# Performance work log

Measured on AMD Instinct MI355X. Metric: run time of the kernel, lower is better.

The kernel has to match this reference:

```python
import jax, jax.numpy as jnp
import numpy as np

N_NODES = 100000
N_EDGES = 1000000
IN_DIM = 64
HID_DIM = 64


def _gcn_conv(x, W, b, rows, cols, deg_inv_sqrt):
    # x: [N, Fin] -> [N, Fout]; rows/cols already include self-loops
    xw = x @ W                                   # [N, Fout]
    norm = deg_inv_sqrt[rows] * deg_inv_sqrt[cols]  # [E+N]
    msg = xw[cols] * norm[:, None]               # gather + scale, [E+N, Fout]
    out = jax.ops.segment_sum(msg, rows, num_segments=x.shape[0])  # scatter-add
    return out + b


def _prelu(x, a):
    return jnp.where(x >= 0, x, a * x)


def _encode(x, edge_index, perm, W1, b1, prelu_a, W2, b2):
    N = x.shape[0]
    loops = jnp.arange(N, dtype=edge_index.dtype)
    rows = jnp.concatenate([edge_index[0], loops])
    cols = jnp.concatenate([edge_index[1], loops])
    deg = jax.ops.segment_sum(jnp.ones_like(rows, dtype=x.dtype), rows, num_segments=N)
    dis = jnp.where(deg > 0, jax.lax.rsqrt(deg), 0.0)

    def enc(feat):
        h = _gcn_conv(feat, W1, b1, rows, cols, dis)
        h = _prelu(h, prelu_a)
        return _gcn_conv(h, W2, b2, rows, cols, dis)

    positive = enc(x)
    negative = enc(x[perm])  # corruption: row permutation of features
    summary = jax.nn.sigmoid(positive.mean(axis=0))
    return positive, negative, summary


def setup_inputs() -> dict:
    key = jax.random.key(0)
    kx, ke, kp, k1, k2 = jax.random.split(key, 5)
    x = jax.random.normal(kx, (N_NODES, IN_DIM), dtype=jnp.float32)
    edge_index = jax.random.randint(ke, (2, N_EDGES), 0, N_NODES, dtype=jnp.int32)
    perm = jax.random.permutation(kp, N_NODES).astype(jnp.int32)
    s1 = 1.0 / np.sqrt(IN_DIM)
    s2 = 1.0 / np.sqrt(HID_DIM)
    W1 = jax.random.uniform(k1, (IN_DIM, HID_DIM), jnp.float32, -s1, s1)
    b1 = jnp.zeros((HID_DIM,), jnp.float32)
    W2 = jax.random.uniform(k2, (HID_DIM, HID_DIM), jnp.float32, -s2, s2)
    b2 = jnp.zeros((HID_DIM,), jnp.float32)
    prelu_a = jnp.float32(0.25)
    return {"x": x, "edge_index": edge_index, "perm": perm,
            "W1": W1, "b1": b1, "prelu_a": prelu_a, "W2": W2, "b2": b2}


def reference(x, edge_index, perm, W1, b1, prelu_a, W2, b2):
    return _encode(x, edge_index, perm, W1, b1, prelu_a, W2, b2)
```

## Files before the change

### kernel.cpp

```cpp
#include <hip/hip_runtime.h>
#include <hip/hip_fp16.h>
#include <math.h>

namespace {

constexpr int NN = 100000;
constexpr int NE = 1000000;
constexpr int D  = 64;

constexpr int RPB_LOG = 8;
constexpr int RPB = 1 << RPB_LOG;
constexpr int NBUK = (NN + RPB - 1) >> RPB_LOG;
constexpr int CAP = 4096;
constexpr int TILE = 2048;
constexpr int NTILES = (NE + TILE - 1) / TILE;

using ushort_t = unsigned short;
typedef __attribute__((ext_vector_type(8))) short short8;
typedef __attribute__((ext_vector_type(4))) float f32x4;

union FragU { uint4 v; short8 s; };

__device__ inline void split2(float f0, float f1, unsigned int& hi, unsigned int& lo) {
    unsigned int u0 = __float_as_uint(f0);
    unsigned int u1 = __float_as_uint(f1);
    hi = (u0 >> 16) | (u1 & 0xffff0000u);
    float l0 = f0 - __uint_as_float(u0 & 0xffff0000u);
    float l1 = f1 - __uint_as_float(u1 & 0xffff0000u);
    lo = (__float_as_uint(l0) >> 16) | (__float_as_uint(l1) & 0xffff0000u);
}

__device__ inline unsigned int packh(float a, float b) {
    union { __half2 h; unsigned int u; } cv;
    cv.h = __float22half2_rn(make_float2(a, b));
    return cv.u;
}

__device__ inline float2 h2f(unsigned int v) {
    union { unsigned int u; __half2 h; } cv;
    cv.u = v;
    return __half22float2(cv.h);
}

__global__ void binw_k(const int* __restrict__ rows, const int* __restrict__ cols,
                       int* __restrict__ bcount, unsigned int* __restrict__ binned, int e,
                       const float* __restrict__ W1, const float* __restrict__ W2,
                       uint4* __restrict__ fb) {
    __shared__ int hist[NBUK];
    __shared__ int gbase[NBUK];
    __shared__ int lofs[NBUK];
    if (blockIdx.x == NTILES) {
        int lane = threadIdx.x;
        if (lane < 64) {
            for (int w = 0; w < 2; ++w) {
                const float* W = (w != 0) ? W2 : W1;
                uint4* out = fb + w * 1024;
                for (int ft = 0; ft < 4; ++ft) {
                    for (int kt = 0; kt < 2; ++kt) {
                        int m  = ft * 16 + (lane & 15);
                        int k0 = kt * 32 + (lane >> 4) * 8;
                        unsigned int hi0, lo0, hi1, lo1, hi2, lo2, hi3, lo3;
                        split2(W[(k0 + 0) * 64 + m], W[(k0 + 1) * 64 + m], hi0, lo0);
                        split2(W[(k0 + 2) * 64 + m], W[(k0 + 3) * 64 + m], hi1, lo1);
                        split2(W[(k0 + 4) * 64 + m], W[(k0 + 5) * 64 + m], hi2, lo2);
                        split2(W[(k0 + 6) * 64 + m], W[(k0 + 7) * 64 + m], hi3, lo3);
                        out[((ft * 2 + kt) * 2 + 0) * 64 + lane] = make_uint4(hi0, hi1, hi2, hi3);
                        out[((ft * 2 + kt) * 2 + 1) * 64 + lane] = make_uint4(lo0, lo1, lo2, lo3);
                    }
                }
            }
        }
        return;
    }
    int base = blockIdx.x * TILE;
    for (int i = threadIdx.x; i < NBUK; i += blockDim.x) {
        hist[i] = 0;
        lofs[i] = 0;
    }
    __syncthreads();
    int r[8];
    int c[8];
    int bk[8];
#pragma unroll
    for (int j = 0; j < 8; ++j) {
        int i = base + j * 256 + threadIdx.x;
        if (i < e) {
            r[j] = rows[i];
            c[j] = cols[i];
            bk[j] = r[j] >> RPB_LOG;
            atomicAdd(&hist[bk[j]], 1);
        } else {
            bk[j] = -1;
        }
    }
    __syncthreads();
    for (int b = threadIdx.x; b < NBUK; b += blockDim.x) {
        int h = hist[b];
        gbase[b] = h ? atomicAdd(&bcount[b], h) : 0;
    }
    __syncthreads();
#pragma unroll
    for (int j = 0; j < 8; ++j) {
        if (bk[j] >= 0) {
            int l = gbase[bk[j]] + atomicAdd(&lofs[bk[j]], 1);
            if (l < CAP) {
                unsigned int v = ((unsigned int)(r[j] & (RPB - 1)) << 17) | (unsigned int)c[j];
                binned[(size_t)bk[j] * CAP + l] = v;
            }
        }
    }
}

__global__ void bucket_sort_k(const unsigned int* __restrict__ binned,
                              const int* __restrict__ bcount,
                              int* __restrict__ scols, int* __restrict__ rowstart,
                              int* __restrict__ deg, float* __restrict__ dis) {
    __shared__ int lcur[RPB];
    __shared__ int srs[RPB];
    __shared__ int wsum[8];
    __shared__ int redpart[8];
    __shared__ int sbase;
    int b = blockIdx.x;
    int row0 = b << RPB_LOG;
    int nrows = min(RPB, NN - row0);
    int cnt = bcount[b];
    const unsigned int* src = binned + (size_t)b * CAP;
    int tid = threadIdx.x;
    int lane = tid & 63;
    int wid = tid >> 6;

    int bv = (tid < NBUK && tid < b) ? bcount[tid] : 0;
    int bs = bv;
#pragma unroll
    for (int off = 1; off < 64; off <<= 1) {
        bs += __shfl_xor(bs, off, 64);
    }
    if (lane == 0) redpart[wid] = bs;
    __syncthreads();
    if (tid == 0) {
        int t = 0;
        for (int w = 0; w < 8; ++w) t += redpart[w];
        sbase = t;
    }
    if (tid < RPB) {
        lcur[tid] = 0;
    }
    __syncthreads();
    int bb = sbase;

    for (int i = tid; i < cnt; i += blockDim.x) {
        atomicAdd(&lcur[src[i] >> 17], 1);
    }
    __syncthreads();
    int d = (tid < nrows) ? lcur[tid] : 0;
    int inc = d;
#pragma unroll
    for (int off = 1; off < 64; off <<= 1) {
        int t = __shfl_up(inc, off);
        if (lane >= off) inc += t;
    }
    if (lane == 63) wsum[wid] = inc;
    __syncthreads();
    int wpre = 0;
    for (int w = 0; w < wid; ++w) wpre += wsum[w];
    int gstart = bb + wpre + inc - d;
    if (tid < nrows) {
        rowstart[row0 + tid] = gstart;
        deg[row0 + tid] = d;
        dis[row0 + tid] = rsqrtf((float)(d + 1));
    }
    __syncthreads();
    if (tid < RPB) {
        srs[tid] = gstart;
        lcur[tid] = 0;
    }
    __syncthreads();
    for (int i = tid; i < cnt; i += blockDim.x) {
        unsigned int v = src[i];
        int rl = (int)(v >> 17);
        int pos = srs[rl] + atomicAdd(&lcur[rl], 1);
        scols[pos] = (int)(v & 0x1FFFFu);
    }
}

__global__ void gemm1_k(const float* __restrict__ in, const uint4* __restrict__ wf,
                        ushort_t* __restrict__ tPN, const int* __restrict__ perm,
                        const float* __restrict__ dis, int n) {
    int lane  = threadIdx.x & 63;
    int wtile = (int)((blockIdx.x * blockDim.x + threadIdx.x) >> 6);
    if (wtile * 16 >= n) return;
    int node = wtile * 16 + (lane & 15);
    int kg   = lane >> 4;

    FragU whi[4][2];
    FragU wlo[4][2];
#pragma unroll
    for (int ft = 0; ft < 4; ++ft) {
#pragma unroll
        for (int kt = 0; kt < 2; ++kt) {
            whi[ft][kt].v = wf[((ft * 2 + kt) * 2 + 0) * 64 + lane];
            wlo[ft][kt].v = wf[((ft * 2 + kt) * 2 + 1) * 64 + lane];
        }
    }

    const float4* xr = (const float4*)in;
    size_t rbase = (size_t)node * 16 + (size_t)(kg * 2);
    int pnode = perm[node];
    size_t pbase = (size_t)pnode * 16 + (size_t)(kg * 2);
    f32x4 accP[4];
    f32x4 accN[4];
#pragma unroll
    for (int ft = 0; ft < 4; ++ft) {
        accP[ft] = f32x4{0.f, 0.f, 0.f, 0.f};
        accN[ft] = f32x4{0.f, 0.f, 0.f, 0.f};
    }
#pragma unroll
    for (int kt = 0; kt < 2; ++kt) {
        float4 a0 = xr[rbase + kt * 8];
        float4 a1 = xr[rbase + kt * 8 + 1];
        float4 g0 = xr[pbase + kt * 8];
        float4 g1 = xr[pbase + kt * 8 + 1];
        unsigned int h0, l0, h1, l1, h2, l2, h3, l3;
        split2(a0.x, a0.y, h0, l0);
        split2(a0.z, a0.w, h1, l1);
        split2(a1.x, a1.y, h2, l2);
        split2(a1.z, a1.w, h3, l3);
        FragU xhiP, xloP;
        xhiP.v = make_uint4(h0, h1, h2, h3);
        xloP.v = make_uint4(l0, l1, l2, l3);
        split2(g0.x, g0.y, h0, l0);
        split2(g0.z, g0.w, h1, l1);
        split2(g1.x, g1.y, h2, l2);
        split2(g1.z, g1.w, h3, l3);
        FragU xhiN, xloN;
        xhiN.v = make_uint4(h0, h1, h2, h3);
        xloN.v = make_uint4(l0, l1, l2, l3);
#pragma unroll
        for (int ft = 0; ft < 4; ++ft) {
            accP[ft] = __builtin_amdgcn_mfma_f32_16x16x32_bf16(whi[ft][kt].s, xhiP.s, accP[ft], 0, 0, 0);
            accP[ft] = __builtin_amdgcn_mfma_f32_16x16x32_bf16(whi[ft][kt].s, xloP.s, accP[ft], 0, 0, 0);
            accP[ft] = __builtin_amdgcn_mfma_f32_16x16x32_bf16(wlo[ft][kt].s, xhiP.s, accP[ft], 0, 0, 0);
            accN[ft] = __builtin_amdgcn_mfma_f32_16x16x32_bf16(whi[ft][kt].s, xhiN.s, accN[ft], 0, 0, 0);
            accN[ft] = __builtin_amdgcn_mfma_f32_16x16x32_bf16(whi[ft][kt].s, xloN.s, accN[ft], 0, 0, 0);
            accN[ft] = __builtin_amdgcn_mfma_f32_16x16x32_bf16(wlo[ft][kt].s, xhiN.s, accN[ft], 0, 0, 0);
        }
    }
    int fo = kg * 4;
    float s = dis[node];
    ushort_t* p = tPN + (size_t)node * 128;
#pragma unroll
    for (int ft = 0; ft < 4; ++ft) {
        uint2 up = make_uint2(packh(s * accP[ft][0], s * accP[ft][1]),
                              packh(s * accP[ft][2], s * accP[ft][3]));
        *(uint2*)(p + ft * 16 + fo) = up;
        uint2 un = make_uint2(packh(s * accN[ft][0], s * accN[ft][1]),
                              packh(s * accN[ft][2], s * accN[ft][3]));
        *(uint2*)(p + 64 + ft * 16 + fo) = un;
    }
}

__global__ void agg_gemm_k(const ushort_t* __restrict__ tIn, ushort_t* __restrict__ tOut,
                           const float* __restrict__ dis,
                           const int* __restrict__ rowstart, const int* __restrict__ deg,
                           const int* __restrict__ scols,
                           const float* __restrict__ bias, const float* __restrict__ prelu_a,
                           const uint4* __restrict__ wf) {
    __shared__ float Hs[2][16][68];
    int tid = threadIdx.x;
    int lane = tid & 63;
    int wv = tid >> 6;
    int row0 = blockIdx.x * 16;
    int hl = lane & 31;
    int half = lane >> 5;
    size_t lofs = (size_t)(half * 64 + hl * 2);
    float aPr = *prelu_a;

    for (int rr = 0; rr < 4; ++rr) {
        int r = row0 + wv * 4 + rr;
        int rs   = __builtin_amdgcn_readfirstlane(r);
        int base = __builtin_amdgcn_readfirstlane(rowstart[rs]);
        int dg   = __builtin_amdgcn_readfirstlane(deg[rs]);
        float dr = dis[rs];
        unsigned int sv = *(const unsigned int*)(tIn + (size_t)rs * 128 + lofs);
        float2 fs = h2f(sv);
        float a0 = fs.x;
        float a1 = fs.y;
        int j = 0;
        for (; j + 4 <= dg; j += 4) {
            int c0 = scols[base + j];
            int c1 = scols[base + j + 1];
            int c2 = scols[base + j + 2];
            int c3 = scols[base + j + 3];
            unsigned int v0 = *(const unsigned int*)(tIn + (size_t)c0 * 128 + lofs);
            unsigned int v1 = *(const unsigned int*)(tIn + (size_t)c1 * 128 + lofs);
            unsigned int v2 = *(const unsigned int*)(tIn + (size_t)c2 * 128 + lofs);
            unsigned int v3 = *(const unsigned int*)(tIn + (size_t)c3 * 128 + lofs);
            float2 f0 = h2f(v0);
            float2 f1 = h2f(v1);
            float2 f2 = h2f(v2);
            float2 f3 = h2f(v3);
            a0 += f0.x + f1.x + f2.x + f3.x;
            a1 += f0.y + f1.y + f2.y + f3.y;
        }
        for (; j < dg; ++j) {
            int c = scols[base + j];
            unsigned int v = *(const unsigned int*)(tIn + (size_t)c * 128 + lofs);
            float2 f = h2f(v);
            a0 += f.x;
            a1 += f.y;
        }
        float2 bv = *(const float2*)(bias + 2 * hl);
        float v0 = fmaf(dr, a0, bv.x);
        float v1 = fmaf(dr, a1, bv.y);
        v0 = v0 >= 0.f ? v0 : aPr * v0;
        v1 = v1 >= 0.f ? v1 : aPr * v1;
        int rl = wv * 4 + rr;
        Hs[half][rl][2 * hl]     = v0;
        Hs[half][rl][2 * hl + 1] = v1;
    }
    __syncthreads();

    int kg = lane >> 4;
    int nd = lane & 15;
    int hsel = wv >> 1;
    int ftb = (wv & 1) * 2;
    FragU whi[2][2];
    FragU wlo[2][2];
#pragma unroll
    for (int f2 = 0; f2 < 2; ++f2) {
#pragma unroll
        for (int kt = 0; kt < 2; ++kt) {
            whi[f2][kt].v = wf[(((ftb + f2) * 2 + kt) * 2 + 0) * 64 + lane];
            wlo[f2][kt].v = wf[(((ftb + f2) * 2 + kt) * 2 + 1) * 64 + lane];
        }
    }
    f32x4 acc[2];
    acc[0] = f32x4{0.f, 0.f, 0.f, 0.f};
    acc[1] = f32x4{0.f, 0.f, 0.f, 0.f};
#pragma unroll
    for (int kt = 0; kt < 2; ++kt) {
        float4 a0 = *(const float4*)&Hs[hsel][nd][kt * 32 + kg * 8];
        float4 a1 = *(const float4*)&Hs[hsel][nd][kt * 32 + kg * 8 + 4];
        unsigned int h0, l0, h1, l1, h2, l2, h3, l3;
        split2(a0.x, a0.y, h0, l0);
        split2(a0.z, a0.w, h1, l1);
        split2(a1.x, a1.y, h2, l2);
        split2(a1.z, a1.w, h3, l3);
        FragU xhi, xlo;
        xhi.v = make_uint4(h0, h1, h2, h3);
        xlo.v = make_uint4(l0, l1, l2, l3);
#pragma unroll
        for (int f2 = 0; f2 < 2; ++f2) {
            acc[f2] = __builtin_amdgcn_mfma_f32_16x16x32_bf16(whi[f2][kt].s, xhi.s, acc[f2], 0, 0, 0);
            acc[f2] = __builtin_amdgcn_mfma_f32_16x16x32_bf16(whi[f2][kt].s, xlo.s, acc[f2], 0, 0, 0);
            acc[f2] = __builtin_amdgcn_mfma_f32_16x16x32_bf16(wlo[f2][kt].s, xhi.s, acc[f2], 0, 0, 0);
        }
    }
    float s = dis[row0 + nd];
    ushort_t* p = tOut + (size_t)(row0 + nd) * 128 + hsel * 64;
    int fo = kg * 4;
#pragma unroll
    for (int f2 = 0; f2 < 2; ++f2) {
        uint2 u = make_uint2(packh(s * acc[f2][0], s * acc[f2][1]),
                             packh(s * acc[f2][2], s * acc[f2][3]));
        *(uint2*)(p + (ftb + f2) * 16 + fo) = u;
    }
}

__global__ void agg_dual_k(const ushort_t* __restrict__ tPN,
                           float* __restrict__ dstP, float* __restrict__ dstN,
                           const float* __restrict__ dis,
                           const int* __restrict__ rowstart, const int* __restrict__ deg,
                           const int* __restrict__ scols,
                           const float* __restrict__ bias, int n) {
    int lane = threadIdx.x & 63;
    int hl = lane & 31;
    int half = lane >> 5;
    int r = blockIdx.x * (blockDim.x >> 6) + (threadIdx.x >> 6);
    if (r >= n) return;
    int rs   = __builtin_amdgcn_readfirstlane(r);
    int base = __builtin_amdgcn_readfirstlane(rowstart[rs]);
    int dg   = __builtin_amdgcn_readfirstlane(deg[rs]);
    float dr = dis[rs];
    size_t lofs = (size_t)(half * 64 + hl * 2);
    unsigned int sv = *(const unsigned int*)(tPN + (size_t)rs * 128 + lofs);
    float2 fs = h2f(sv);
    float a0 = fs.x;
    float a1 = fs.y;
    int j = 0;
    for (; j + 4 <= dg; j += 4) {
        int c0 = scols[base + j];
        int c1 = scols[base + j + 1];
        int c2 = scols[base + j + 2];
        int c3 = scols[base + j + 3];
        unsigned int v0 = *(const unsigned int*)(tPN + (size_t)c0 * 128 + lofs);
        unsigned int v1 = *(const unsigned int*)(tPN + (size_t)c1 * 128 + lofs);
        unsigned int v2 = *(const unsigned int*)(tPN + (size_t)c2 * 128 + lofs);
        unsigned int v3 = *(const unsigned int*)(tPN + (size_t)c3 * 128 + lofs);
        float2 f0 = h2f(v0);
        float2 f1 = h2f(v1);
        float2 f2 = h2f(v2);
        float2 f3 = h2f(v3);
        a0 += f0.x + f1.x + f2.x + f3.x;
        a1 += f0.y + f1.y + f2.y + f3.y;
    }
    for (; j < dg; ++j) {
        int c = scols[base + j];
        unsigned int v = *(const unsigned int*)(tPN + (size_t)c * 128 + lofs);
        float2 f = h2f(v);
        a0 += f.x;
        a1 += f.y;
    }
    float2 bv = *(const float2*)(bias + 2 * hl);
    float v0 = fmaf(dr, a0, bv.x);
    float v1 = fmaf(dr, a1, bv.y);
    float* dst = half ? dstN : dstP;
    *(float2*)(dst + (size_t)rs * D + 2 * hl) = float2{v0, v1};
}

__global__ void summary_partial_k(const float* __restrict__ pos, float* __restrict__ acc, int n) {
    __shared__ float red[4][64];
    int lane = threadIdx.x & 63;
    int wv = threadIdx.x >> 6;
    int wave = (blockIdx.x * blockDim.x + threadIdx.x) >> 6;
    int nw = (gridDim.x * blockDim.x) >> 6;
    float s0 = 0.f, s1 = 0.f, s2 = 0.f, s3 = 0.f;
    int r = wave;
    for (; r + 3 * nw < n; r += 4 * nw) {
        s0 += pos[(size_t)r * D + lane];
        s1 += pos[(size_t)(r + nw) * D + lane];
        s2 += pos[(size_t)(r + 2 * nw) * D + lane];
        s3 += pos[(size_t)(r + 3 * nw) * D + lane];
    }
    for (; r < n; r += nw) {
        s0 += pos[(size_t)r * D + lane];
    }
    red[wv][lane] = (s0 + s1) + (s2 + s3);
    __syncthreads();
    if (wv == 0) {
        float t = (red[0][lane] + red[1][lane]) + (red[2][lane] + red[3][lane]);
        atomicAdd(&acc[lane], t);
    }
}

__global__ void summary_final_k(const float* __restrict__ acc, float* __restrict__ out, int n) {
    int f = threadIdx.x;
    if (f < D) {
        float m = acc[f] / (float)n;
        out[f] = 1.f / (1.f + expf(-m));
    }
}

}

extern "C" void kernel_launch(void* const* d_in, const int* in_sizes, int n_in,
                              void* d_out, int out_size, void* d_ws, size_t ws_size,
                              hipStream_t stream) {
    (void)in_sizes; (void)n_in; (void)out_size; (void)ws_size;
    const float* x       = (const float*)d_in[0];
    const int*   ei      = (const int*)  d_in[1];
    const int*   perm    = (const int*)  d_in[2];
    const float* W1      = (const float*)d_in[3];
    const float* b1      = (const float*)d_in[4];
    const float* prelu_a = (const float*)d_in[5];
    const float* W2      = (const float*)d_in[6];
    const float* b2      = (const float*)d_in[7];

    float* outP = (float*)d_out;
    float* outN = outP + (size_t)NN * D;
    float* outS = outN + (size_t)NN * D;

    const int* erows = ei;
    const int* ecols = ei + NE;

    char* ws = (char*)d_ws;
    size_t off = 0;
    auto alloc = [&](size_t bytes) {
        void* p = ws + off;
        off = (off + bytes + 255) & ~(size_t)255;
        return p;
    };
    int*      deg      = (int*)     alloc((size_t)NN * 4);
    float*    dis      = (float*)   alloc((size_t)NN * 4);
    int*      rowstart = (int*)     alloc((size_t)NN * 4);
    int*      bcount   = (int*)     alloc((size_t)NBUK * 4);
    float*    acc      = (float*)   alloc((size_t)D * 4);
    unsigned int* binned = (unsigned int*)alloc((size_t)NBUK * CAP * 4);
    int*      scols    = (int*)     alloc((size_t)NE * 4);
    ushort_t* tPN      = (ushort_t*)alloc((size_t)NN * 128 * 2);
    ushort_t* tPN2     = (ushort_t*)alloc((size_t)NN * 128 * 2);
    uint4*    wfrag    = (uint4*)   alloc((size_t)2 * 1024 * 16);

    hipMemsetAsync(bcount, 0, (size_t)((char*)acc - (char*)bcount) + (size_t)D * 4, stream);

    binw_k<<<NTILES + 1, 256, 0, stream>>>(erows, ecols, bcount, binned, NE, W1, W2, wfrag);
    bucket_sort_k<<<NBUK, 512, 0, stream>>>(binned, bcount, scols, rowstart, deg, dis);

    gemm1_k<<<(NN / 16 + 3) / 4, 256, 0, stream>>>(x, wfrag, tPN, perm, dis, NN);

    agg_gemm_k<<<NN / 16, 256, 0, stream>>>(tPN, tPN2, dis, rowstart, deg, scols,
                                            b1, prelu_a, wfrag + 1024);

    agg_dual_k<<<(NN + 3) / 4, 256, 0, stream>>>(tPN2, outP, outN, dis, rowstart, deg,
                                                 scols, b2, NN);

    summary_partial_k<<<512, 256, 0, stream>>>(outP, acc, NN);
    summary_final_k<<<1, 64, 0, stream>>>(acc, outS, NN);
}
```

Baseline: 253.8 us.

## Fuse first GEMM into edge-binning kernel, move source-degree scaling into aggregation

The first-layer X@W1 GEMM (positive and permuted) now runs as extra blocks of the edge-binning kernel, so it no longer waits on the bucket sort and one launch goes away. Because dis is not yet known at that point, the source-side normalisation is moved into the first aggregation, which now loads dis[c] for every neighbour and applies it with an FMA. W1 fragments are built in registers per wave rather than read from a prebuilt buffer. The cost is an extra random gather of dis per edge in the aggregation, and redundant per-wave W1 splitting.

```diff
diff --git a/kernel.cpp b/kernel.cpp
--- a/kernel.cpp
+++ b/kernel.cpp
@@ -14,6 +14,7 @@
 constexpr int CAP = 4096;
 constexpr int TILE = 2048;
 constexpr int NTILES = (NE + TILE - 1) / TILE;
+constexpr int G1B = (NN / 16 + 3) / 4;
 
 using ushort_t = unsigned short;
 typedef __attribute__((ext_vector_type(8))) short short8;
@@ -42,37 +43,124 @@
     return __half22float2(cv.h);
 }
 
-__global__ void binw_k(const int* __restrict__ rows, const int* __restrict__ cols,
-                       int* __restrict__ bcount, unsigned int* __restrict__ binned, int e,
-                       const float* __restrict__ W1, const float* __restrict__ W2,
-                       uint4* __restrict__ fb) {
+__device__ inline void build_wfrags(const float* __restrict__ W, int lane,
+                                    FragU (&whi)[4][2], FragU (&wlo)[4][2]) {
+#pragma unroll
+    for (int ft = 0; ft < 4; ++ft) {
+#pragma unroll
+        for (int kt = 0; kt < 2; ++kt) {
+            int m  = ft * 16 + (lane & 15);
+            int k0 = kt * 32 + (lane >> 4) * 8;
+            unsigned int hi0, lo0, hi1, lo1, hi2, lo2, hi3, lo3;
+            split2(W[(k0 + 0) * 64 + m], W[(k0 + 1) * 64 + m], hi0, lo0);
+            split2(W[(k0 + 2) * 64 + m], W[(k0 + 3) * 64 + m], hi1, lo1);
+            split2(W[(k0 + 4) * 64 + m], W[(k0 + 5) * 64 + m], hi2, lo2);
+            split2(W[(k0 + 6) * 64 + m], W[(k0 + 7) * 64 + m], hi3, lo3);
+            whi[ft][kt].v = make_uint4(hi0, hi1, hi2, hi3);
+            wlo[ft][kt].v = make_uint4(lo0, lo1, lo2, lo3);
+        }
+    }
+}
+
+__global__ void pre_k(const int* __restrict__ rows, const int* __restrict__ cols,
+                      int* __restrict__ bcount, unsigned int* __restrict__ binned, int e,
+                      const float* __restrict__ W1, const float* __restrict__ W2,
+                      uint4* __restrict__ fb,
+                      const float* __restrict__ x, const int* __restrict__ perm,
+                      ushort_t* __restrict__ tPN) {
     __shared__ int hist[NBUK];
     __shared__ int gbase[NBUK];
     __shared__ int lofs[NBUK];
-    if (blockIdx.x == NTILES) {
+    int bid = blockIdx.x;
+
+    if (bid > NTILES) {
+        int lane  = threadIdx.x & 63;
+        int wtile = (bid - NTILES - 1) * 4 + (threadIdx.x >> 6);
+        if (wtile * 16 >= NN) return;
+        int node = wtile * 16 + (lane & 15);
+        int kg   = lane >> 4;
+
+        FragU whi[4][2];
+        FragU wlo[4][2];
+        build_wfrags(W1, lane, whi, wlo);
+
+        const float4* xr = (const float4*)x;
+        size_t rbase = (size_t)node * 16 + (size_t)(kg * 2);
+        int pnode = perm[node];
+        size_t pbase = (size_t)pnode * 16 + (size_t)(kg * 2);
+        f32x4 accP[4];
+        f32x4 accN[4];
+#pragma unroll
+        for (int ft = 0; ft < 4; ++ft) {
+            accP[ft] = f32x4{0.f, 0.f, 0.f, 0.f};
+            accN[ft] = f32x4{0.f, 0.f, 0.f, 0.f};
+        }
+#pragma unroll
+        for (int kt = 0; kt < 2; ++kt) {
+            float4 a0 = xr[rbase + kt * 8];
+            float4 a1 = xr[rbase + kt * 8 + 1];
+            float4 g0 = xr[pbase + kt * 8];
+            float4 g1 = xr[pbase + kt * 8 + 1];
+            unsigned int h0, l0, h1, l1, h2, l2, h3, l3;
+            split2(a0.x, a0.y, h0, l0);
+            split2(a0.z, a0.w, h1, l1);
+            split2(a1.x, a1.y, h2, l2);
+            split2(a1.z, a1.w, h3, l3);
+            FragU xhiP, xloP;
+            xhiP.v = make_uint4(h0, h1, h2, h3);
+            xloP.v = make_uint4(l0, l1, l2, l3);
+            split2(g0.x, g0.y, h0, l0);
+            split2(g0.z, g0.w, h1, l1);
+            split2(g1.x, g1.y, h2, l2);
+            split2(g1.z, g1.w, h3, l3);
+            FragU xhiN, xloN;
+            xhiN.v = make_uint4(h0, h1, h2, h3);
+            xloN.v = make_uint4(l0, l1, l2, l3);
+#pragma unroll
+            for (int ft = 0; ft < 4; ++ft) {
+                accP[ft] = __builtin_amdgcn_mfma_f32_16x16x32_bf16(whi[ft][kt].s, xhiP.s, accP[ft], 0, 0, 0);
+                accP[ft] = __builtin_amdgcn_mfma_f32_16x16x32_bf16(whi[ft][kt].s, xloP.s, accP[ft], 0, 0, 0);
+                accP[ft] = __builtin_amdgcn_mfma_f32_16x16x32_bf16(wlo[ft][kt].s, xhiP.s, accP[ft], 0, 0, 0);
+                accN[ft] = __builtin_amdgcn_mfma_f32_16x16x32_bf16(whi[ft][kt].s, xhiN.s, accN[ft], 0, 0, 0);
+                accN[ft] = __builtin_amdgcn_mfma_f32_16x16x32_bf16(whi[ft][kt].s, xloN.s, accN[ft], 0, 0, 0);
+                accN[ft] = __builtin_amdgcn_mfma_f32_16x16x32_bf16(wlo[ft][kt].s, xhiN.s, accN[ft], 0, 0, 0);
+            }
+        }
+        int fo = kg * 4;
+        ushort_t* p = tPN + (size_t)node * 128;
+#pragma unroll
+        for (int ft = 0; ft < 4; ++ft) {
+            uint2 up = make_uint2(packh(accP[ft][0], accP[ft][1]),
+                                  packh(accP[ft][2], accP[ft][3]));
+            *(uint2*)(p + ft * 16 + fo) = up;
+            uint2 un = make_uint2(packh(accN[ft][0], accN[ft][1]),
+                                  packh(accN[ft][2], accN[ft][3]));
+            *(uint2*)(p + 64 + ft * 16 + fo) = un;
+        }
+        return;
+    }
+
+    if (bid == NTILES) {
         int lane = threadIdx.x;
         if (lane < 64) {
-            for (int w = 0; w < 2; ++w) {
-                const float* W = (w != 0) ? W2 : W1;
-                uint4* out = fb + w * 1024;
-                for (int ft = 0; ft < 4; ++ft) {
-                    for (int kt = 0; kt < 2; ++kt) {
-                        int m  = ft * 16 + (lane & 15);
-                        int k0 = kt * 32 + (lane >> 4) * 8;
-                        unsigned int hi0, lo0, hi1, lo1, hi2, lo2, hi3, lo3;
-                        split2(W[(k0 + 0) * 64 + m], W[(k0 + 1) * 64 + m], hi0, lo0);
-                        split2(W[(k0 + 2) * 64 + m], W[(k0 + 3) * 64 + m], hi1, lo1);
-                        split2(W[(k0 + 4) * 64 + m], W[(k0 + 5) * 64 + m], hi2, lo2);
-                        split2(W[(k0 + 6) * 64 + m], W[(k0 + 7) * 64 + m], hi3, lo3);
-                        out[((ft * 2 + kt) * 2 + 0) * 64 + lane] = make_uint4(hi0, hi1, hi2, hi3);
-                        out[((ft * 2 + kt) * 2 + 1) * 64 + lane] = make_uint4(lo0, lo1, lo2, lo3);
-                    }
+            for (int ft = 0; ft < 4; ++ft) {
+                for (int kt = 0; kt < 2; ++kt) {
+                    int m  = ft * 16 + (lane & 15);
+                    int k0 = kt * 32 + (lane >> 4) * 8;
+                    unsigned int hi0, lo0, hi1, lo1, hi2, lo2, hi3, lo3;
+                    split2(W2[(k0 + 0) * 64 + m], W2[(k0 + 1) * 64 + m], hi0, lo0);
+                    split2(W2[(k0 + 2) * 64 + m], W2[(k0 + 3) * 64 + m], hi1, lo1);
+                    split2(W2[(k0 + 4) * 64 + m], W2[(k0 + 5) * 64 + m], hi2, lo2);
+                    split2(W2[(k0 + 6) * 64 + m], W2[(k0 + 7) * 64 + m], hi3, lo3);
+                    fb[((ft * 2 + kt) * 2 + 0) * 64 + lane] = make_uint4(hi0, hi1, hi2, hi3);
+                    fb[((ft * 2 + kt) * 2 + 1) * 64 + lane] = make_uint4(lo0, lo1, lo2, lo3);
                 }
             }
         }
         return;
     }
-    int base = blockIdx.x * TILE;
+
+    int base = bid * TILE;
     for (int i = threadIdx.x; i < NBUK; i += blockDim.x) {
         hist[i] = 0;
         lofs[i] = 0;
@@ -183,82 +271,6 @@
     }
 }
 
-__global__ void gemm1_k(const float* __restrict__ in, const uint4* __restrict__ wf,
-                        ushort_t* __restrict__ tPN, const int* __restrict__ perm,
-                        const float* __restrict__ dis, int n) {
-    int lane  = threadIdx.x & 63;
-    int wtile = (int)((blockIdx.x * blockDim.x + threadIdx.x) >> 6);
-    if (wtile * 16 >= n) return;
-    int node = wtile * 16 + (lane & 15);
-    int kg   = lane >> 4;
-
-    FragU whi[4][2];
-    FragU wlo[4][2];
-#pragma unroll
-    for (int ft = 0; ft < 4; ++ft) {
-#pragma unroll
-        for (int kt = 0; kt < 2; ++kt) {
-            whi[ft][kt].v = wf[((ft * 2 + kt) * 2 + 0) * 64 + lane];
-            wlo[ft][kt].v = wf[((ft * 2 + kt) * 2 + 1) * 64 + lane];
-        }
-    }
-
-    const float4* xr = (const float4*)in;
-    size_t rbase = (size_t)node * 16 + (size_t)(kg * 2);
-    int pnode = perm[node];
-    size_t pbase = (size_t)pnode * 16 + (size_t)(kg * 2);
-    f32x4 accP[4];
-    f32x4 accN[4];
-#pragma unroll
-    for (int ft = 0; ft < 4; ++ft) {
-        accP[ft] = f32x4{0.f, 0.f, 0.f, 0.f};
-        accN[ft] = f32x4{0.f, 0.f, 0.f, 0.f};
-    }
-#pragma unroll
-    for (int kt = 0; kt < 2; ++kt) {
-        float4 a0 = xr[rbase + kt * 8];
-        float4 a1 = xr[rbase + kt * 8 + 1];
-        float4 g0 = xr[pbase + kt * 8];
-        float4 g1 = xr[pbase + kt * 8 + 1];
-        unsigned int h0, l0, h1, l1, h2, l2, h3, l3;
-        split2(a0.x, a0.y, h0, l0);
-        split2(a0.z, a0.w, h1, l1);
-        split2(a1.x, a1.y, h2, l2);
-        split2(a1.z, a1.w, h3, l3);
-        FragU xhiP, xloP;
-        xhiP.v = make_uint4(h0, h1, h2, h3);
-        xloP.v = make_uint4(l0, l1, l2, l3);
-        split2(g0.x, g0.y, h0, l0);
-        split2(g0.z, g0.w, h1, l1);
-        split2(g1.x, g1.y, h2, l2);
-        split2(g1.z, g1.w, h3, l3);
-        FragU xhiN, xloN;
-        xhiN.v = make_uint4(h0, h1, h2, h3);
-        xloN.v = make_uint4(l0, l1, l2, l3);
-#pragma unroll
-        for (int ft = 0; ft < 4; ++ft) {
-            accP[ft] = __builtin_amdgcn_mfma_f32_16x16x32_bf16(whi[ft][kt].s, xhiP.s, accP[ft], 0, 0, 0);
-            accP[ft] = __builtin_amdgcn_mfma_f32_16x16x32_bf16(whi[ft][kt].s, xloP.s, accP[ft], 0, 0, 0);
-            accP[ft] = __builtin_amdgcn_mfma_f32_16x16x32_bf16(wlo[ft][kt].s, xhiP.s, accP[ft], 0, 0, 0);
-            accN[ft] = __builtin_amdgcn_mfma_f32_16x16x32_bf16(whi[ft][kt].s, xhiN.s, accN[ft], 0, 0, 0);
-            accN[ft] = __builtin_amdgcn_mfma_f32_16x16x32_bf16(whi[ft][kt].s, xloN.s, accN[ft], 0, 0, 0);
-            accN[ft] = __builtin_amdgcn_mfma_f32_16x16x32_bf16(wlo[ft][kt].s, xhiN.s, accN[ft], 0, 0, 0);
-        }
-    }
-    int fo = kg * 4;
-    float s = dis[node];
-    ushort_t* p = tPN + (size_t)node * 128;
-#pragma unroll
-    for (int ft = 0; ft < 4; ++ft) {
-        uint2 up = make_uint2(packh(s * accP[ft][0], s * accP[ft][1]),
-                              packh(s * accP[ft][2], s * accP[ft][3]));
-        *(uint2*)(p + ft * 16 + fo) = up;
-        uint2 un = make_uint2(packh(s * accN[ft][0], s * accN[ft][1]),
-                              packh(s * accN[ft][2], s * accN[ft][3]));
-        *(uint2*)(p + 64 + ft * 16 + fo) = un;
-    }
-}
-
 __global__ void agg_gemm_k(const ushort_t* __restrict__ tIn, ushort_t* __restrict__ tOut,
                            const float* __restrict__ dis,
                            const int* __restrict__ rowstart, const int* __restrict__ deg,
@@ -283,14 +295,18 @@
         float dr = dis[rs];
         unsigned int sv = *(const unsigned int*)(tIn + (size_t)rs * 128 + lofs);
         float2 fs = h2f(sv);
-        float a0 = fs.x;
-        float a1 = fs.y;
+        float a0 = dr * fs.x;
+        float a1 = dr * fs.y;
         int j = 0;
         for (; j + 4 <= dg; j += 4) {
             int c0 = scols[base + j];
             int c1 = scols[base + j + 1];
             int c2 = scols[base + j + 2];
             int c3 = scols[base + j + 3];
+            float d0 = dis[c0];
+            float d1 = dis[c1];
+            float d2 = dis[c2];
+            float d3 = dis[c3];
             unsigned int v0 = *(const unsigned int*)(tIn + (size_t)c0 * 128 + lofs);
             unsigned int v1 = *(const unsigned int*)(tIn + (size_t)c1 * 128 + lofs);
             unsigned int v2 = *(const unsigned int*)(tIn + (size_t)c2 * 128 + lofs);
@@ -299,15 +315,22 @@
             float2 f1 = h2f(v1);
             float2 f2 = h2f(v2);
             float2 f3 = h2f(v3);
-            a0 += f0.x + f1.x + f2.x + f3.x;
-            a1 += f0.y + f1.y + f2.y + f3.y;
+            a0 = fmaf(d0, f0.x, a0);
+            a1 = fmaf(d0, f0.y, a1);
+            a0 = fmaf(d1, f1.x, a0);
+            a1 = fmaf(d1, f1.y, a1);
+            a0 = fmaf(d2, f2.x, a0);
+            a1 = fmaf(d2, f2.y, a1);
+            a0 = fmaf(d3, f3.x, a0);
+            a1 = fmaf(d3, f3.y, a1);
         }
         for (; j < dg; ++j) {
             int c = scols[base + j];
+            float dc = dis[c];
             unsigned int v = *(const unsigned int*)(tIn + (size_t)c * 128 + lofs);
             float2 f = h2f(v);
-            a0 += f.x;
-            a1 += f.y;
+            a0 = fmaf(dc, f.x, a0);
+            a1 = fmaf(dc, f.y, a1);
         }
         float2 bv = *(const float2*)(bias + 2 * hl);
         float v0 = fmaf(dr, a0, bv.x);
@@ -489,17 +512,16 @@
     int*      scols    = (int*)     alloc((size_t)NE * 4);
     ushort_t* tPN      = (ushort_t*)alloc((size_t)NN * 128 * 2);
     ushort_t* tPN2     = (ushort_t*)alloc((size_t)NN * 128 * 2);
-    uint4*    wfrag    = (uint4*)   alloc((size_t)2 * 1024 * 16);
+    uint4*    wfrag    = (uint4*)   alloc((size_t)1024 * 16);
 
     hipMemsetAsync(bcount, 0, (size_t)((char*)acc - (char*)bcount) + (size_t)D * 4, stream);
 
-    binw_k<<<NTILES + 1, 256, 0, stream>>>(erows, ecols, bcount, binned, NE, W1, W2, wfrag);
+    pre_k<<<NTILES + 1 + G1B, 256, 0, stream>>>(erows, ecols, bcount, binned, NE,
+                                                W1, W2, wfrag, x, perm, tPN);
     bucket_sort_k<<<NBUK, 512, 0, stream>>>(binned, bcount, scols, rowstart, deg, dis);
 
-    gemm1_k<<<(NN / 16 + 3) / 4, 256, 0, stream>>>(x, wfrag, tPN, perm, dis, NN);
-
     agg_gemm_k<<<NN / 16, 256, 0, stream>>>(tPN, tPN2, dis, rowstart, deg, scols,
-                                            b1, prelu_a, wfrag + 1024);
+                                            b1, prelu_a, wfrag);
 
     agg_dual_k<<<(NN + 3) / 4, 256, 0, stream>>>(tPN2, outP, outN, dis, rowstart, deg,
                                                  scols, b2, NN);
```

Result: no change. 254.7 us (+0.3%).
